# Kernel optimization log

Hardware: AMD Instinct MI355X
Metric: run time of the kernel (lower is better)

The kernel has to match this reference:

```python
import jax, jax.numpy as jnp
import numpy as np
from jax import lax

B, H, W, C = 8, 128, 128, 256
HEADS, DHEAD = 8, 32
INNER = HEADS * DHEAD  # == C, required by pos_emb reshape


def setup_inputs() -> dict:
    key = jax.random.key(0)
    ks = jax.random.split(key, 12)
    s = 0.02
    return {
        "x_in": jax.random.normal(ks[0], (B, H, W, C), jnp.float32),
        "Wq": jax.random.normal(ks[1], (INNER, C), jnp.float32) * s,
        "Wk": jax.random.normal(ks[2], (INNER, C), jnp.float32) * s,
        "Wv": jax.random.normal(ks[3], (INNER, C), jnp.float32) * s,
        "rescale": jnp.ones((HEADS, 1, 1), jnp.float32),
        "Wp": jax.random.normal(ks[4], (C, INNER), jnp.float32) * s,
        "bp": jnp.zeros((C,), jnp.float32),
        "Wc1": jax.random.normal(ks[5], (INNER, INNER, 3, 3), jnp.float32) * s,
        "bc1": jnp.zeros((INNER,), jnp.float32),
        "Wc2": jax.random.normal(ks[6], (INNER, INNER, 3, 3), jnp.float32) * s,
        "bc2": jnp.zeros((INNER,), jnp.float32),
    }


def _l2norm(x, axis=-1, eps=1e-12):
    n = jnp.sqrt(jnp.sum(x * x, axis=axis, keepdims=True))
    return x / jnp.maximum(n, eps)


def _conv(x, w, b):
    y = lax.conv_general_dilated(x, w, (1, 1), 'SAME',
                                 dimension_numbers=('NCHW', 'OIHW', 'NCHW'))
    return y + b[None, :, None, None]


def reference(x_in, Wq, Wk, Wv, rescale, Wp, bp, Wc1, bc1, Wc2, bc2):
    b, h, w, c = x_in.shape
    n = h * w
    x = x_in.reshape(b, n, c)
    q_inp = x @ Wq.T  # [b, n, inner]
    k_inp = x @ Wk.T
    v_inp = x @ Wv.T

    def heads(t):  # b n (h d) -> b h d n  (already transposed)
        return t.reshape(b, n, HEADS, DHEAD).transpose(0, 2, 3, 1)

    q = _l2norm(heads(q_inp))  # [b, heads, d, n], normalized over n
    k = _l2norm(heads(k_inp))
    v = heads(v_inp)  # [b, heads, d, n]

    attn = jnp.einsum('bhdn,bhen->bhde', k, q) * rescale  # [b, heads, d, d]
    attn = jax.nn.softmax(attn, axis=-1)
    xo = jnp.einsum('bhde,bhen->bhdn', attn, v)  # [b, heads, d, n]
    xo = xo.transpose(0, 3, 1, 2).reshape(b, n, INNER)  # b n (heads d)
    out_c = (xo @ Wp.T + bp).reshape(b, h, w, c)

    vp = v_inp.reshape(b, h, w, INNER).transpose(0, 3, 1, 2)  # NCHW
    p = _conv(vp, Wc1, bc1)
    p = jax.nn.gelu(p, approximate=False)
    p = _conv(p, Wc2, bc2)
    out_p = p.transpose(0, 2, 3, 1)  # b h w c
    return out_c, out_p
```

## Files before the change

kernel.cpp:

```cpp
#include <hip/hip_runtime.h>
#include <cstdint>

#define DEV __device__ __forceinline__

typedef __bf16 bf16x8 __attribute__((ext_vector_type(8)));
typedef float f32x4 __attribute__((ext_vector_type(4)));
typedef unsigned int u32;
typedef unsigned short u16;

DEV u16 f2bf(float f) {
  u32 u = __builtin_bit_cast(u32, f);
  u += 0x7fffu + ((u >> 16) & 1u);
  return (u16)(u >> 16);
}
DEV float bf2f(u16 b) { return __builtin_bit_cast(float, (u32)b << 16); }

DEV void gload16(const u16* g, u16* l) {
  __builtin_amdgcn_global_load_lds(
      (const __attribute__((address_space(1))) u32*)g,
      (__attribute__((address_space(3))) u32*)(uintptr_t)l, 16, 0, 0);
}

DEV void border_body(u16* __restrict__ p, int idx) {
  int pix = idx >> 5, c8 = (idx & 31) << 3;
  int b = pix / 516, r = pix % 516;
  int x, y;
  if (r < 130)      { y = 0;   x = r; }
  else if (r < 260) { y = 129; x = r - 130; }
  else if (r < 388) { x = 0;   y = r - 259; }
  else              { x = 129; y = r - 387; }
  u16* dst = p + (((long)b * 130 + y) * 130 + x) * 256 + c8;
  *reinterpret_cast<uint4*>(dst) = uint4{0, 0, 0, 0};
}

__global__ void cvt_f32_bf16(const float* __restrict__ in, u16* __restrict__ out, int n4) {
  int i = blockIdx.x * blockDim.x + threadIdx.x;
  if (i >= n4) return;
  float4 v = reinterpret_cast<const float4*>(in)[i];
  ushort4 o;
  o.x = f2bf(v.x); o.y = f2bf(v.y); o.z = f2bf(v.z); o.w = f2bf(v.w);
  reinterpret_cast<ushort4*>(out)[i] = o;
}

__global__ void prep(const float* __restrict__ Wq, const float* __restrict__ Wk,
                     const float* __restrict__ Wv, const float* __restrict__ Wc1,
                     const float* __restrict__ Wc2, u16* __restrict__ wqkv,
                     u16* __restrict__ wc1r, u16* __restrict__ wc2r, u16* __restrict__ vpad) {
  const int blk = blockIdx.x, t = threadIdx.x;
  if (blk < 192) {
    const float* src = blk < 64 ? Wq : (blk < 128 ? Wk : Wv);
    u16* dst = wqkv + (blk < 64 ? 0 : (blk < 128 ? 65536 : 131072));
    const int i = (blk & 63) * 256 + t;
    float4 v = reinterpret_cast<const float4*>(src)[i];
    ushort4 o;
    o.x = f2bf(v.x); o.y = f2bf(v.y); o.z = f2bf(v.z); o.w = f2bf(v.w);
    reinterpret_cast<ushort4*>(dst)[i] = o;
  } else if (blk < 4800) {
    const int q = blk - 192;
    const float* w = q < 2304 ? Wc1 : Wc2;
    u16* dst = q < 2304 ? wc1r : wc2r;
    const int j = (q % 2304) * 256 + t;
    const int oc = j / 2304, r = j - oc * 2304;
    const int kt = r >> 6, c_lo = r & 63;
    const int cg = kt / 9, slab = kt - cg * 9;
    const int ic = cg * 64 + c_lo;
    dst[j] = f2bf(w[(oc * 256 + ic) * 9 + slab]);
  } else {
    const int idx = (blk - 4800) * 256 + t;
    if (idx < 8 * 516 * 32) border_body(vpad, idx);
  }
}

template <int CONV, int KTOT, int EPI, int PERB, int SWZ>
__global__ __launch_bounds__(512, 1) void mm8(
    const u16* __restrict__ A, const u16* __restrict__ Bt,
    const float* __restrict__ bias, void* __restrict__ out,
    u16* __restrict__ vp) {
  extern __shared__ u16 lds[];
  constexpr int NKT = KTOT / 64;
  constexpr int NITER = NKT / 2;
  const int tid = threadIdx.x;
  const int wave = tid >> 6, lane = tid & 63;
  const int wr = wave >> 2, wcid = wave & 3;
  const int lrow = lane & 15, lk = lane >> 4;
  int bid = (int)blockIdx.x;
  int tile, colbase;
  if (SWZ == 1) {
    const int xcd = bid & 7, k = bid >> 3;
    tile = (xcd + ((k >> 5) << 3)) * 32 + (k & 31);
    colbase = 0;
  } else if (SWZ == 2) {
    const int xcd = bid & 7, s = bid >> 3;
    const int r = s / 3;
    tile = xcd * 64 + r;
    colbase = (s - r * 3) * 256;
  } else {
    tile = (bid & 7) * 64 + (bid >> 3);
    colbase = 0;
  }
  const long rowbase = (long)tile * 256;
  const int bimg = tile >> 6;
  const int y0 = (tile & 63) * 2;
  const u16* BT = PERB ? Bt + (long)bimg * 65536 : Bt;

  const int rh0 = tid >> 3;
  const int sg0 = (tid & 7) ^ (rh0 & 7);
  const u16* laneA0 = A + rh0 * 256 + sg0 * 8;
  const u16* laneA1 = laneA0 + 64 * 256;
  const u16* laneB0 = BT + (long)rh0 * KTOT + sg0 * 8;
  const u16* laneB1 = laneB0 + (long)64 * KTOT;
  u16* ldsl = lds + wave * 512;

  auto STAGE = [&](int kt, int isB, int half, int bufq) {
    int uofs;
    if (isB) {
      uofs = (colbase + half * 128) * KTOT + kt * 64;
    } else if (CONV == 1) {
      const int cg = kt / 9;
      const int slab = kt - cg * 9;
      const int ky = slab / 3 - 1, kx = slab - (slab / 3) * 3 - 1;
      uofs = ((bimg * 130 + y0 + half + 1 + ky) * 130 + 1 + kx) * 256 + cg * 64;
    } else if (CONV == 2) {
      uofs = ((bimg * 130 + y0 + half + 1) * 130 + 1) * 256 + kt * 64;
    } else {
      uofs = (int)(rowbase + half * 128) * 256 + kt * 64;
    }
    u16* l = ldsl + (isB ? 32768 : 0) + bufq * 16384 + half * 8192;
    gload16((isB ? laneB0 : laneA0) + uofs, l);
    gload16((isB ? laneB1 : laneA1) + uofs, l + 4096);
  };

  f32x4 acc[8][4] = {};
  bf16x8 bq[4][2];

  STAGE(0, 1, 0, 0); STAGE(0, 1, 1, 0);
  STAGE(0, 0, 0, 0); STAGE(0, 0, 1, 0);
  STAGE(1, 1, 0, 1); STAGE(1, 1, 1, 1);
  asm volatile("s_waitcnt vmcnt(4)" ::: "memory");
  __builtin_amdgcn_s_barrier();
  __builtin_amdgcn_sched_barrier(0);

  for (int it = 0; it < NITER; ++it) {
    const int u0 = 2 * it;
#pragma unroll
    for (int ph = 0; ph < 8; ++ph) {
      constexpr int S_ISB[8]  = {0, 0, 1, 1, 0, 0, 1, 1};
      constexpr int S_HALF[8] = {0, 1, 0, 1, 0, 1, 0, 1};
      constexpr int S_BUF[8]  = {1, 1, 0, 0, 0, 0, 1, 1};
      constexpr int S_DT[8]   = {1, 1, 2, 2, 2, 2, 3, 3};
      const int cbuf = ph >> 2, quad = ph & 3;
      if (quad == 0) {
#pragma unroll
        for (int nf = 0; nf < 4; ++nf)
#pragma unroll
          for (int ks = 0; ks < 2; ++ks) {
            const int n = wcid * 64 + nf * 16 + lrow;
            const int slot = (ks * 4 + lk) ^ (n & 7);
            bq[nf][ks] = *reinterpret_cast<const bf16x8*>(&lds[32768 + cbuf * 16384 + n * 64 + slot * 8]);
          }
      }
      bf16x8 aq[2][2];
#pragma unroll
      for (int mf = 0; mf < 2; ++mf)
#pragma unroll
        for (int ks = 0; ks < 2; ++ks) {
          const int r = wr * 128 + quad * 32 + mf * 16 + lrow;
          const int slot = (ks * 4 + lk) ^ (r & 7);
          aq[mf][ks] = *reinterpret_cast<const bf16x8*>(&lds[cbuf * 16384 + r * 64 + slot * 8]);
        }
      int st = u0 + S_DT[ph];
      if (st > NKT - 1) st = NKT - 1;
      STAGE(st, S_ISB[ph], S_HALF[ph], S_BUF[ph]);
      if (quad == 0)
        asm volatile("s_waitcnt lgkmcnt(8)" ::: "memory");
      __builtin_amdgcn_s_barrier();
      asm volatile("s_waitcnt lgkmcnt(0)" ::: "memory");
      __builtin_amdgcn_sched_barrier(0);
      __builtin_amdgcn_s_setprio(1);
#pragma unroll
      for (int mf = 0; mf < 2; ++mf)
#pragma unroll
        for (int nf = 0; nf < 4; ++nf)
#pragma unroll
          for (int ks = 0; ks < 2; ++ks)
            acc[quad * 2 + mf][nf] = __builtin_amdgcn_mfma_f32_16x16x32_bf16(
                aq[mf][ks], bq[nf][ks], acc[quad * 2 + mf][nf], 0, 0, 0);
      __builtin_amdgcn_s_setprio(0);
      __builtin_amdgcn_sched_barrier(0);
      if (quad == 3)
        asm volatile("s_waitcnt vmcnt(4)" ::: "memory");
      __builtin_amdgcn_s_barrier();
      __builtin_amdgcn_sched_barrier(0);
    }
  }

  const int r0 = (lane >> 4) * 4;
  const int occ = lane & 15;
#pragma unroll
  for (int M = 0; M < 8; ++M) {
#pragma unroll
    for (int nf = 0; nf < 4; ++nf) {
      const int col = wcid * 64 + nf * 16 + occ;
#pragma unroll
      for (int i = 0; i < 4; ++i) {
        const int p = wr * 128 + M * 16 + r0 + i;
        float v = acc[M][nf][i];
        if (EPI == 0) {
          const long rowpix = rowbase + p;
          const int gcol = colbase + col;
          if (gcol < 512) {
            reinterpret_cast<u16*>(out)[rowpix * 512 + gcol] = f2bf(v);
          } else {
            const int b = (int)(rowpix >> 14), rem = (int)(rowpix & 16383);
            vp[(((long)b * 130 + (rem >> 7) + 1) * 130 + (rem & 127) + 1) * 256 + (gcol - 512)] = f2bf(v);
          }
        } else if (EPI == 1) {
          reinterpret_cast<float*>(out)[(rowbase + p) * 256 + col] = v + bias[col];
        } else {
          v += bias[col];
          v = 0.5f * v * (1.0f + erff(v * 0.70710678118654752f));
          const int y = y0 + (p >> 7), x = p & 127;
          reinterpret_cast<u16*>(out)[(((long)bimg * 130 + y + 1) * 130 + x + 1) * 256 + col] = f2bf(v);
        }
      }
    }
  }
}

__global__ __launch_bounds__(256) void gram_mfma(const u16* __restrict__ qkv,
                                                 float* __restrict__ G,
                                                 float* __restrict__ norm2) {
  __shared__ __align__(16) u16 kT[2][32][40];
  __shared__ __align__(16) u16 qT[2][32][40];
  __shared__ float redq[256][4];
  __shared__ float redk[256][4];
  const int nc = blockIdx.x;
  const int bh = blockIdx.y;
  const int b = bh >> 3, h = bh & 7;
  const int t = threadIdx.x;
  const int wave = t >> 6, lane = t & 63;
  const int mh = wave >> 1, nh = wave & 1;
  const int r = t >> 3, cg = (t & 7) * 4;
  const long n0 = (long)b * 16384 + (long)nc * 4096;
  const u16* qp = qkv + n0 * 512 + h * 32;
  const u16* kp = qp + 256;
  f32x4 acc = {0.f, 0.f, 0.f, 0.f};
  float sq[4] = {0, 0, 0, 0}, sk[4] = {0, 0, 0, 0};

  ushort4 pq[4], pk[4];
#pragma unroll
  for (int j = 0; j < 4; ++j) {
    pq[j] = *reinterpret_cast<const ushort4*>(qp + (long)(j * 32 + r) * 512 + cg);
    pk[j] = *reinterpret_cast<const ushort4*>(kp + (long)(j * 32 + r) * 512 + cg);
  }

  for (int s4 = 0; s4 < 32; ++s4) {
#pragma unroll
    for (int c = 0; c < 4; ++c) {
      const int s = s4 * 4 + c;
      const int buf = s & 1;
      kT[buf][cg + 0][r] = pk[c].x; kT[buf][cg + 1][r] = pk[c].y;
      kT[buf][cg + 2][r] = pk[c].z; kT[buf][cg + 3][r] = pk[c].w;
      qT[buf][cg + 0][r] = pq[c].x; qT[buf][cg + 1][r] = pq[c].y;
      qT[buf][cg + 2][r] = pq[c].z; qT[buf][cg + 3][r] = pq[c].w;
      float f;
      f = bf2f(pq[c].x); sq[0] += f * f;
      f = bf2f(pq[c].y); sq[1] += f * f;
      f = bf2f(pq[c].z); sq[2] += f * f;
      f = bf2f(pq[c].w); sq[3] += f * f;
      f = bf2f(pk[c].x); sk[0] += f * f;
      f = bf2f(pk[c].y); sk[1] += f * f;
      f = bf2f(pk[c].z); sk[2] += f * f;
      f = bf2f(pk[c].w); sk[3] += f * f;
      if (s + 4 < 128) {
        pq[c] = *reinterpret_cast<const ushort4*>(qp + (long)((s + 4) * 32 + r) * 512 + cg);
        pk[c] = *reinterpret_cast<const ushort4*>(kp + (long)((s + 4) * 32 + r) * 512 + cg);
      }
      __syncthreads();
      bf16x8 af = *reinterpret_cast<const bf16x8*>(&kT[buf][mh * 16 + (lane & 15)][(lane >> 4) * 8]);
      bf16x8 bf = *reinterpret_cast<const bf16x8*>(&qT[buf][nh * 16 + (lane & 15)][(lane >> 4) * 8]);
      acc = __builtin_amdgcn_mfma_f32_16x16x32_bf16(af, bf, acc, 0, 0, 0);
    }
  }

  float* gp = G + (long)bh * 1024 + (mh * 16 + (lane >> 4) * 4) * 32 + nh * 16 + (lane & 15);
#pragma unroll
  for (int i = 0; i < 4; ++i) atomicAdd(gp + i * 32, acc[i]);

  __syncthreads();
#pragma unroll
  for (int j = 0; j < 4; ++j) { redq[t][j] = sq[j]; redk[t][j] = sk[j]; }
  __syncthreads();
  if (t < 64) {
    const int qk = t >> 5;
    const int colid = t & 31;
    const int cgi = colid >> 2, j = colid & 3;
    float s = 0.f;
#pragma unroll
    for (int r2 = 0; r2 < 32; ++r2)
      s += qk ? redk[r2 * 8 + cgi][j] : redq[r2 * 8 + cgi][j];
    atomicAdd(&norm2[b * 512 + qk * 256 + h * 32 + colid], s);
  }
}

__global__ void attn_softmax(const float* __restrict__ G, const float* __restrict__ norm2,
                             const float* __restrict__ rescale, float* __restrict__ attn) {
  const int bh = blockIdx.x;
  const int b = bh >> 3, h = bh & 7;
  const int t = threadIdx.x;
  __shared__ float iqs[32], iks[32];
  if (t < 32) {
    iqs[t] = 1.0f / fmaxf(sqrtf(norm2[b * 512 + h * 32 + t]), 1e-12f);
    iks[t] = 1.0f / fmaxf(sqrtf(norm2[b * 512 + 256 + h * 32 + t]), 1e-12f);
  }
  __syncthreads();
  if (t < 32) {
    const float rs = rescale[h];
    const float ikd = iks[t] * rs;
    const float* gp = G + ((long)bh * 32 + t) * 32;
    float l[32];
    float mx = -1e30f;
#pragma unroll
    for (int e = 0; e < 32; ++e) {
      l[e] = gp[e] * ikd * iqs[e];
      mx = fmaxf(mx, l[e]);
    }
    float s = 0.f;
#pragma unroll
    for (int e = 0; e < 32; ++e) {
      l[e] = expf(l[e] - mx);
      s += l[e];
    }
    const float inv = 1.0f / s;
    float* op = attn + ((long)bh * 32 + t) * 32;
#pragma unroll
    for (int e = 0; e < 32; ++e) op[e] = l[e] * inv;
  }
}

__global__ __launch_bounds__(256) void weff_border(const float* __restrict__ Wp,
                                                   const float* __restrict__ attn,
                                                   u16* __restrict__ weff,
                                                   u16* __restrict__ p1pad) {
  const int blk = blockIdx.x;
  const int t = threadIdx.x;
  if (blk < 64) {
    __shared__ float A[32][33];
    const int b = blk >> 3, h = blk & 7;
    const float* ap = attn + (long)blk * 1024;
    for (int j = t; j < 1024; j += 256) A[j >> 5][j & 31] = ap[j];
    __syncthreads();
    const float* wrow = Wp + (long)t * 256 + h * 32;
    float w[32];
#pragma unroll
    for (int d = 0; d < 32; ++d) w[d] = wrow[d];
    u16* orow = weff + ((long)b * 256 + t) * 256 + h * 32;
#pragma unroll
    for (int e = 0; e < 32; ++e) {
      float s = 0.f;
#pragma unroll
      for (int d = 0; d < 32; ++d) s += w[d] * A[d][e];
      orow[e] = f2bf(s);
    }
  } else {
    const int idx = (blk - 64) * 256 + t;
    if (idx < 8 * 516 * 32) border_body(p1pad, idx);
  }
}

extern "C" void kernel_launch(void* const* d_in, const int* in_sizes, int n_in,
                              void* d_out, int out_size, void* d_ws, size_t ws_size,
                              hipStream_t stream) {
  const float* x = (const float*)d_in[0];
  const float* Wq = (const float*)d_in[1];
  const float* Wk = (const float*)d_in[2];
  const float* Wv = (const float*)d_in[3];
  const float* resc = (const float*)d_in[4];
  const float* Wp = (const float*)d_in[5];
  const float* bp = (const float*)d_in[6];
  const float* Wc1 = (const float*)d_in[7];
  const float* bc1 = (const float*)d_in[8];
  const float* Wc2 = (const float*)d_in[9];
  const float* bc2 = (const float*)d_in[10];

  char* ws = (char*)d_ws;
  u16* qkv   = (u16*)(ws + 0L);
  u16* p1pad = (u16*)(ws + 0L);
  u16* vpad  = (u16*)(ws + 134217728L);
  u16* xb    = (u16*)(ws + 203440128L);
  u16* wqkv  = (u16*)(ws + 270548992L);
  u16* wc1r  = (u16*)(ws + 270942208L);
  u16* wc2r  = (u16*)(ws + 272121856L);
  u16* weff  = (u16*)(ws + 273301504L);
  float* norm2 = (float*)(ws + 274350080L);
  float* G     = (float*)(ws + 274366464L);
  float* attn  = (float*)(ws + 274628608L);

  float* out_c = (float*)d_out;
  float* out_p = out_c + 33554432L;

  hipMemsetAsync(norm2, 0, 16384 + 262144, stream);

  cvt_f32_bf16<<<32768, 256, 0, stream>>>(x, xb, 8388608);
  prep<<<5316, 256, 0, stream>>>(Wq, Wk, Wv, Wc1, Wc2, wqkv, wc1r, wc2r, vpad);

  mm8<0, 256, 0, 0, 2><<<1536, 512, 131072, stream>>>(xb, wqkv, nullptr, qkv, vpad);

  gram_mfma<<<dim3(4, 64), 256, 0, stream>>>(qkv, G, norm2);
  attn_softmax<<<64, 64, 0, stream>>>(G, norm2, resc, attn);
  weff_border<<<580, 256, 0, stream>>>(Wp, attn, weff, p1pad);

  mm8<2, 256, 1, 1, 0><<<512, 512, 131072, stream>>>(vpad, weff, bp, out_c, nullptr);

  mm8<1, 2304, 2, 0, 1><<<512, 512, 131072, stream>>>(vpad, wc1r, bc1, p1pad, nullptr);
  mm8<1, 2304, 1, 0, 1><<<512, 512, 131072, stream>>>(p1pad, wc2r, bc2, out_p, nullptr);
}
```

Baseline: 556.3 us.

## Triple-buffer B tiles and prefetch B fragments one group ahead in mm8

The GEMM main loop now keeps three LDS buffers for the B operand instead of two, raising dynamic LDS from 128 KiB to 160 KiB. B fragments are loaded into two register sets (bqA/bqB), one quarter per phase, for the next k-group while the current group's MFMAs run. This replaces the bulk B-fragment load and lgkmcnt wait at the start of each group. The goal is to hide LDS read latency and smooth global-to-LDS staging, at the cost of more registers and LDS, and it keeps occupancy at one block per CU.

```diff
diff --git a/kernel.cpp b/kernel.cpp
--- a/kernel.cpp
+++ b/kernel.cpp
@@ -131,34 +131,38 @@
   };
 
   f32x4 acc[8][4] = {};
-  bf16x8 bq[4][2];
+  bf16x8 bqA[4][2], bqB[4][2];
 
   STAGE(0, 1, 0, 0); STAGE(0, 1, 1, 0);
+  STAGE(1, 1, 0, 1); STAGE(1, 1, 1, 1);
   STAGE(0, 0, 0, 0); STAGE(0, 0, 1, 0);
-  STAGE(1, 1, 0, 1); STAGE(1, 1, 1, 1);
+  STAGE(2, 1, 0, 2); STAGE(2, 1, 1, 2);
   asm volatile("s_waitcnt vmcnt(4)" ::: "memory");
   __builtin_amdgcn_s_barrier();
   __builtin_amdgcn_sched_barrier(0);
-
+#pragma unroll
+  for (int nf = 0; nf < 4; ++nf)
+#pragma unroll
+    for (int ks = 0; ks < 2; ++ks) {
+      const int n = wcid * 64 + nf * 16 + lrow;
+      const int slot = (ks * 4 + lk) ^ (n & 7);
+      bqA[nf][ks] = *reinterpret_cast<const bf16x8*>(&lds[32768 + n * 64 + slot * 8]);
+    }
+
+  int bt0 = 0;
   for (int it = 0; it < NITER; ++it) {
     const int u0 = 2 * it;
+    const int btA = bt0;
+    const int btB = btA == 2 ? 0 : btA + 1;
+    const int btC = btB == 2 ? 0 : btB + 1;
+    const int stA[2] = {u0 + 1 < NKT ? u0 + 1 : NKT - 1, u0 + 2 < NKT ? u0 + 2 : NKT - 1};
+    const int stB[2] = {u0 + 3 < NKT ? u0 + 3 : NKT - 1, u0 + 4 < NKT ? u0 + 4 : NKT - 1};
+    const int sbB[2] = {btA, btB};
+    const int rb[2]  = {u0 + 1 < NKT ? btB : btA,
+                        u0 + 2 < NKT ? btC : btB};
 #pragma unroll
     for (int ph = 0; ph < 8; ++ph) {
-      constexpr int S_ISB[8]  = {0, 0, 1, 1, 0, 0, 1, 1};
-      constexpr int S_HALF[8] = {0, 1, 0, 1, 0, 1, 0, 1};
-      constexpr int S_BUF[8]  = {1, 1, 0, 0, 0, 0, 1, 1};
-      constexpr int S_DT[8]   = {1, 1, 2, 2, 2, 2, 3, 3};
-      const int cbuf = ph >> 2, quad = ph & 3;
-      if (quad == 0) {
-#pragma unroll
-        for (int nf = 0; nf < 4; ++nf)
-#pragma unroll
-          for (int ks = 0; ks < 2; ++ks) {
-            const int n = wcid * 64 + nf * 16 + lrow;
-            const int slot = (ks * 4 + lk) ^ (n & 7);
-            bq[nf][ks] = *reinterpret_cast<const bf16x8*>(&lds[32768 + cbuf * 16384 + n * 64 + slot * 8]);
-          }
-      }
+      const int grp = ph >> 2, quad = ph & 3;
       bf16x8 aq[2][2];
 #pragma unroll
       for (int mf = 0; mf < 2; ++mf)
@@ -166,13 +170,20 @@
         for (int ks = 0; ks < 2; ++ks) {
           const int r = wr * 128 + quad * 32 + mf * 16 + lrow;
           const int slot = (ks * 4 + lk) ^ (r & 7);
-          aq[mf][ks] = *reinterpret_cast<const bf16x8*>(&lds[cbuf * 16384 + r * 64 + slot * 8]);
+          aq[mf][ks] = *reinterpret_cast<const bf16x8*>(&lds[grp * 16384 + r * 64 + slot * 8]);
         }
-      int st = u0 + S_DT[ph];
-      if (st > NKT - 1) st = NKT - 1;
-      STAGE(st, S_ISB[ph], S_HALF[ph], S_BUF[ph]);
-      if (quad == 0)
-        asm volatile("s_waitcnt lgkmcnt(8)" ::: "memory");
+      {
+        const int n = wcid * 64 + quad * 16 + lrow;
+#pragma unroll
+        for (int ks = 0; ks < 2; ++ks) {
+          const int slot = (ks * 4 + lk) ^ (n & 7);
+          const bf16x8 v = *reinterpret_cast<const bf16x8*>(
+              &lds[32768 + rb[grp] * 16384 + n * 64 + slot * 8]);
+          if (grp) bqA[quad][ks] = v; else bqB[quad][ks] = v;
+        }
+      }
+      if (quad < 2) STAGE(stA[grp], 0, quad, grp ^ 1);
+      else          STAGE(stB[grp], 1, quad - 2, sbB[grp]);
       __builtin_amdgcn_s_barrier();
       asm volatile("s_waitcnt lgkmcnt(0)" ::: "memory");
       __builtin_amdgcn_sched_barrier(0);
@@ -184,7 +195,7 @@
 #pragma unroll
           for (int ks = 0; ks < 2; ++ks)
             acc[quad * 2 + mf][nf] = __builtin_amdgcn_mfma_f32_16x16x32_bf16(
-                aq[mf][ks], bq[nf][ks], acc[quad * 2 + mf][nf], 0, 0, 0);
+                aq[mf][ks], grp ? bqB[nf][ks] : bqA[nf][ks], acc[quad * 2 + mf][nf], 0, 0, 0);
       __builtin_amdgcn_s_setprio(0);
       __builtin_amdgcn_sched_barrier(0);
       if (quad == 3)
@@ -192,6 +203,7 @@
       __builtin_amdgcn_s_barrier();
       __builtin_amdgcn_sched_barrier(0);
     }
+    bt0 = btC;
   }
 
   const int r0 = (lane >> 4) * 4;
@@ -404,14 +416,14 @@
   cvt_f32_bf16<<<32768, 256, 0, stream>>>(x, xb, 8388608);
   prep<<<5316, 256, 0, stream>>>(Wq, Wk, Wv, Wc1, Wc2, wqkv, wc1r, wc2r, vpad);
 
-  mm8<0, 256, 0, 0, 2><<<1536, 512, 131072, stream>>>(xb, wqkv, nullptr, qkv, vpad);
+  mm8<0, 256, 0, 0, 2><<<1536, 512, 163840, stream>>>(xb, wqkv, nullptr, qkv, vpad);
 
   gram_mfma<<<dim3(4, 64), 256, 0, stream>>>(qkv, G, norm2);
   attn_softmax<<<64, 64, 0, stream>>>(G, norm2, resc, attn);
   weff_border<<<580, 256, 0, stream>>>(Wp, attn, weff, p1pad);
 
-  mm8<2, 256, 1, 1, 0><<<512, 512, 131072, stream>>>(vpad, weff, bp, out_c, nullptr);
-
-  mm8<1, 2304, 2, 0, 1><<<512, 512, 131072, stream>>>(vpad, wc1r, bc1, p1pad, nullptr);
-  mm8<1, 2304, 1, 0, 1><<<512, 512, 131072, stream>>>(p1pad, wc2r, bc2, out_p, nullptr);
-}
+  mm8<2, 256, 1, 1, 0><<<512, 512, 163840, stream>>>(vpad, weff, bp, out_c, nullptr);
+
+  mm8<1, 2304, 2, 0, 1><<<512, 512, 163840, stream>>>(vpad, wc1r, bc1, p1pad, nullptr);
+  mm8<1, 2304, 1, 0, 1><<<512, 512, 163840, stream>>>(p1pad, wc2r, bc2, out_p, nullptr);
+}
```

After: 582.7 us. 4.7% more time.

## Replace large-tile mm8 with small 128x128 gemm kernel for K=256 GEMMs

Applied to the files above, without the earlier changes.

Adds a new 256-thread gemm128 kernel with 128x128 output tiles, 32-wide K steps and small static LDS, and uses it for the QKV projection and the out_c projection instead of the 512-thread, 128KB-LDS mm8 kernel. These GEMMs have only K=256, so the big pipelined tiles had few K iterations and low occupancy. The new kernel runs many more small blocks concurrently to hide latency. In exchange it has no double buffering, two barriers per K step and less data reuse per block.

```diff
diff --git a/kernel.cpp b/kernel.cpp
--- a/kernel.cpp
+++ b/kernel.cpp
@@ -71,6 +71,86 @@
   }
 }
 
+template <int EPI>
+__global__ __launch_bounds__(256) void gemm128(
+    const u16* __restrict__ A, const u16* __restrict__ Bt,
+    const float* __restrict__ bias, void* __restrict__ out,
+    u16* __restrict__ vp) {
+  __shared__ __align__(16) u16 As[128 * 32];
+  __shared__ __align__(16) u16 Bs[128 * 32];
+  const int tid = threadIdx.x;
+  const int wave = tid >> 6, lane = tid & 63;
+  const int wr = (wave >> 1) * 64, wc = (wave & 1) * 64;
+  const int lrow = lane & 15, kofs = (lane >> 4) * 8;
+  constexpr int NCT = (EPI == 0) ? 6 : 2;
+  const int bid = (int)blockIdx.x;
+  const int xcd = bid & 7, s = bid >> 3;
+  const int rt = s / NCT, ct = s - rt * NCT;
+  const int tile = xcd * 128 + rt;
+  const int colbase = ct * 128;
+  const long rowbase = (long)tile * 128;
+  const int bimg = tile >> 7;
+  const int yrow = tile & 127;
+
+  const int rh = tid >> 2, sg = tid & 3;
+  const u16* laneB = Bt + ((EPI == 1) ? (long)bimg * 65536 : 0) +
+                     (long)(colbase + rh) * 256 + sg * 8;
+  const u16* laneA;
+  if (EPI == 0) laneA = A + (rowbase + rh) * 256 + sg * 8;
+  else          laneA = A + (((long)bimg * 130 + yrow + 1) * 130 + rh + 1) * 256 + sg * 8;
+  u16* asl = As + wave * 512;
+  u16* bsl = Bs + wave * 512;
+
+  f32x4 acc[4][4] = {};
+
+  for (int k0 = 0; k0 < 256; k0 += 32) {
+    __syncthreads();
+    gload16(laneA + k0, asl);
+    gload16(laneA + 64 * 256 + k0, asl + 2048);
+    gload16(laneB + k0, bsl);
+    gload16(laneB + 64 * 256 + k0, bsl + 2048);
+    __syncthreads();
+    bf16x8 af[4], bfv[4];
+#pragma unroll
+    for (int m = 0; m < 4; ++m)
+      af[m] = *reinterpret_cast<const bf16x8*>(&As[(wr + m * 16 + lrow) * 32 + kofs]);
+#pragma unroll
+    for (int n = 0; n < 4; ++n)
+      bfv[n] = *reinterpret_cast<const bf16x8*>(&Bs[(wc + n * 16 + lrow) * 32 + kofs]);
+#pragma unroll
+    for (int m = 0; m < 4; ++m)
+#pragma unroll
+      for (int n = 0; n < 4; ++n)
+        acc[m][n] = __builtin_amdgcn_mfma_f32_16x16x32_bf16(af[m], bfv[n], acc[m][n], 0, 0, 0);
+  }
+
+  const int r0 = (lane >> 4) * 4;
+  const int occ = lane & 15;
+#pragma unroll
+  for (int m = 0; m < 4; ++m) {
+#pragma unroll
+    for (int n = 0; n < 4; ++n) {
+      const int lcol = wc + n * 16 + occ;
+      const int col = colbase + lcol;
+#pragma unroll
+      for (int i = 0; i < 4; ++i) {
+        const long row = rowbase + wr + m * 16 + r0 + i;
+        float v = acc[m][n][i];
+        if (EPI == 0) {
+          if (col < 512) {
+            reinterpret_cast<u16*>(out)[row * 512 + col] = f2bf(v);
+          } else {
+            const int b = (int)(row >> 14), rem = (int)(row & 16383);
+            vp[(((long)b * 130 + (rem >> 7) + 1) * 130 + (rem & 127) + 1) * 256 + (col - 512)] = f2bf(v);
+          }
+        } else {
+          reinterpret_cast<float*>(out)[row * 256 + col] = v + bias[col];
+        }
+      }
+    }
+  }
+}
+
 template <int CONV, int KTOT, int EPI, int PERB, int SWZ>
 __global__ __launch_bounds__(512, 1) void mm8(
     const u16* __restrict__ A, const u16* __restrict__ Bt,
@@ -89,11 +169,6 @@
     const int xcd = bid & 7, k = bid >> 3;
     tile = (xcd + ((k >> 5) << 3)) * 32 + (k & 31);
     colbase = 0;
-  } else if (SWZ == 2) {
-    const int xcd = bid & 7, s = bid >> 3;
-    const int r = s / 3;
-    tile = xcd * 64 + r;
-    colbase = (s - r * 3) * 256;
   } else {
     tile = (bid & 7) * 64 + (bid >> 3);
     colbase = 0;
@@ -205,16 +280,7 @@
       for (int i = 0; i < 4; ++i) {
         const int p = wr * 128 + M * 16 + r0 + i;
         float v = acc[M][nf][i];
-        if (EPI == 0) {
-          const long rowpix = rowbase + p;
-          const int gcol = colbase + col;
-          if (gcol < 512) {
-            reinterpret_cast<u16*>(out)[rowpix * 512 + gcol] = f2bf(v);
-          } else {
-            const int b = (int)(rowpix >> 14), rem = (int)(rowpix & 16383);
-            vp[(((long)b * 130 + (rem >> 7) + 1) * 130 + (rem & 127) + 1) * 256 + (gcol - 512)] = f2bf(v);
-          }
-        } else if (EPI == 1) {
+        if (EPI == 1) {
           reinterpret_cast<float*>(out)[(rowbase + p) * 256 + col] = v + bias[col];
         } else {
           v += bias[col];
@@ -404,13 +470,13 @@
   cvt_f32_bf16<<<32768, 256, 0, stream>>>(x, xb, 8388608);
   prep<<<5316, 256, 0, stream>>>(Wq, Wk, Wv, Wc1, Wc2, wqkv, wc1r, wc2r, vpad);
 
-  mm8<0, 256, 0, 0, 2><<<1536, 512, 131072, stream>>>(xb, wqkv, nullptr, qkv, vpad);
+  gemm128<0><<<6144, 256, 0, stream>>>(xb, wqkv, nullptr, qkv, vpad);
 
   gram_mfma<<<dim3(4, 64), 256, 0, stream>>>(qkv, G, norm2);
   attn_softmax<<<64, 64, 0, stream>>>(G, norm2, resc, attn);
   weff_border<<<580, 256, 0, stream>>>(Wp, attn, weff, p1pad);
 
-  mm8<2, 256, 1, 1, 0><<<512, 512, 131072, stream>>>(vpad, weff, bp, out_c, nullptr);
+  gemm128<1><<<2048, 256, 0, stream>>>(vpad, weff, bp, out_c, nullptr);
 
   mm8<1, 2304, 2, 0, 1><<<512, 512, 131072, stream>>>(vpad, wc1r, bc1, p1pad, nullptr);
   mm8<1, 2304, 1, 0, 1><<<512, 512, 131072, stream>>>(p1pad, wc2r, bc2, out_p, nullptr);
```

After: 576.7 us. +3.7%, slower.
